# Kernel tuning notes

Measured on AMD Instinct MI355X. Metric: run time of the kernel, lower is better.

The kernel has to match this reference:

```python
import jax, jax.numpy as jnp
import numpy as np

NF, NX, GROUP_SIZE = 8192, 2048, 64
N_GROUPS = NX // GROUP_SIZE  # pad = 0 since NX % GROUP_SIZE == 0


def setup_inputs() -> dict:
    key = jax.random.key(0)
    k1, k2, k3, k4, k5 = jax.random.split(key, 5)
    x = jax.random.normal(k1, (4, 2048, NX), dtype=jnp.float32)
    packed = jax.random.randint(k2, (NF, NX // 2), 0, 256, dtype=jnp.int32)
    scales = jax.random.uniform(k3, (NF, N_GROUPS), dtype=jnp.float32)
    zeros = jax.random.randint(k4, (NF, N_GROUPS), 0, 16, dtype=jnp.int32)
    bias = jax.random.normal(k5, (NF,), dtype=jnp.float32)
    return {"x": x, "packed": packed, "scales": scales, "zeros": zeros, "bias": bias}


def _dequantize(packed, scales, zeros):
    # packed: [nf, nx//2] bytes, two int4 nibbles per byte (low nibble first)
    low = packed & 15
    high = (packed >> 4) & 15
    # interleave: q[:, 0::2] = low, q[:, 1::2] = high
    q = jnp.stack([low, high], axis=-1).reshape(NF, NX).astype(jnp.float32)
    q = q.reshape(NF, N_GROUPS, GROUP_SIZE)
    W = (q - zeros.astype(jnp.float32)[:, :, None]) * scales[:, :, None]
    return W.reshape(NF, NX)  # [nf, nx]


def reference(x, packed, scales, zeros, bias):
    W = _dequantize(packed, scales, zeros).astype(x.dtype)  # [nf, nx]
    size_out = x.shape[:-1] + (NF,)
    out = jnp.matmul(x.reshape(-1, NX), W.T) + bias  # addmm
    return out.reshape(size_out)
```

## Files before the change

kernel.cpp:

```cpp
#include <hip/hip_runtime.h>
#include <stdint.h>

#define NF 8192
#define NX 2048
#define MROWS 8192
#define NGROUPS 32
#define NSTEP 64

typedef unsigned short u16;
typedef __bf16 bf16x8 __attribute__((ext_vector_type(8)));
typedef float f32x4 __attribute__((ext_vector_type(4)));

#define AS1 __attribute__((address_space(1)))
#define AS3 __attribute__((address_space(3)))

__device__ __forceinline__ void glds16(const void* g, void* l) {
    __builtin_amdgcn_global_load_lds((AS1 void*)(uintptr_t)g,
                                     (AS3 void*)(uintptr_t)l, 16, 0, 0);
}

__device__ __forceinline__ u16 f2bf(float f) {
    unsigned u = __float_as_uint(f);
    return (u16)((u + 0x7FFFu + ((u >> 16) & 1u)) >> 16);
}

__global__ void dequant_kernel(const int* __restrict__ packed,
                               const float* __restrict__ scales,
                               const int* __restrict__ zeros,
                               uint32_t* __restrict__ W2) {
    int tid = blockIdx.x * blockDim.x + threadIdx.x;
    int f = tid >> 10;
    int i = tid & 1023;
    int g = f * NGROUPS + (i >> 5);
    int p = packed[tid];
    float s = scales[g];
    float z = (float)zeros[g];
    float w0 = ((float)(p & 15) - z) * s;
    float w1 = ((float)((p >> 4) & 15) - z) * s;
    W2[tid] = (uint32_t)f2bf(w0) | ((uint32_t)f2bf(w1) << 16);
}

__global__ void cvt_kernel(const float4* __restrict__ x, ushort4* __restrict__ y) {
    int i = blockIdx.x * blockDim.x + threadIdx.x;
    float4 v = x[i];
    ushort4 o;
    o.x = f2bf(v.x); o.y = f2bf(v.y); o.z = f2bf(v.z); o.w = f2bf(v.w);
    y[i] = o;
}


#define BAR    __builtin_amdgcn_s_barrier()
#define LGKM4  asm volatile("s_waitcnt lgkmcnt(4)" ::: "memory")
#define LGKM0  asm volatile("s_waitcnt lgkmcnt(0)" ::: "memory")
#define VMCNT6 asm volatile("s_waitcnt vmcnt(6)" ::: "memory")
#define VMCNT0 asm volatile("s_waitcnt vmcnt(0)" ::: "memory")
#define FENCE  __builtin_amdgcn_sched_barrier(0)

#define LD8(off) (*(const bf16x8*)(smem + (off)))

#define STAGE6(REG, S) do { \
    const char* _sa = srcA + (size_t)(S) * 64; \
    const char* _sb = srcB + (size_t)(S) * 64; \
    glds16(_sa,          smem + (REG) + t16); \
    glds16(_sa + 262144, smem + (REG) + 4096  + t16); \
    glds16(_sa + 524288, smem + (REG) + 8192  + t16); \
    glds16(_sa + 786432, smem + (REG) + 12288 + t16); \
    glds16(_sb,          smem + (REG) + 16384 + t16); \
    glds16(_sb + 262144, smem + (REG) + 20480 + t16); \
} while (0)

__global__ __launch_bounds__(256, 2)
void gemm_kernel(const u16* __restrict__ A, const u16* __restrict__ B,
                 const float* __restrict__ bias, float* __restrict__ C) {
    __shared__ __align__(16) char smem[73728];

    const int t = threadIdx.x;

    const int bid = blockIdx.x;
    const int xcd = bid & 7;
    const int local = bid >> 3;
    const int super = local >> 7;
    const int r = local & 127;
    const int by = xcd * 4 + super * 2 + (r & 1);
    const int bx = r >> 1;
    const int rowA0 = by * 256;
    const int rowB0 = bx * 128;

    const int t16 = t * 16;
    const int kslot = (t & 3) ^ ((t >> 3) & 3);
    const char* srcA = (const char*)A + (size_t)(rowA0 + (t >> 2)) * 4096 + kslot * 16;
    const char* srcB = (const char*)B + (size_t)(rowB0 + (t >> 2)) * 4096 + kslot * 16;

    const int lane = t & 63;
    const int wv = t >> 6;
    const int wm = wv >> 1;
    const int wn = wv & 1;
    const int l15 = lane & 15;
    const int quad = lane >> 4;
    const int uX = ((((l15 >> 1) & 3) ^ quad)) << 4;
    const int aOff = (wm * 128 + l15) * 64 + uX;
    const int bOff = 16384 + (wn * 64 + l15) * 64 + uX;

    f32x4 acc[8][4];
#pragma unroll
    for (int i = 0; i < 8; ++i)
#pragma unroll
        for (int j = 0; j < 4; ++j) acc[i][j] = {0.f, 0.f, 0.f, 0.f};

    bf16x8 a[8], b[4];

    STAGE6(0,     0);
    STAGE6(24576, 1);
    VMCNT6;

    int regC = 0, regN = 24576, regT = 49152;

#pragma unroll 1
    for (int s = 0; s < NSTEP; ++s) {
        FENCE; BAR; FENCE;
#pragma unroll
        for (int i = 0; i < 4; ++i) a[i] = LD8(regC + aOff + i * 1024);
#pragma unroll
        for (int j = 0; j < 4; ++j) b[j] = LD8(regC + bOff + j * 1024);
        FENCE;
#pragma unroll
        for (int i = 4; i < 8; ++i) a[i] = LD8(regC + aOff + i * 1024);
        if (s + 2 < NSTEP) STAGE6(regT, s + 2);
        FENCE; LGKM4; FENCE;
        __builtin_amdgcn_s_setprio(1);
#pragma unroll
        for (int i = 0; i < 4; ++i)
#pragma unroll
            for (int j = 0; j < 4; ++j)
                acc[i][j] = __builtin_amdgcn_mfma_f32_16x16x32_bf16(a[i], b[j], acc[i][j], 0, 0, 0);
        __builtin_amdgcn_s_setprio(0);
        FENCE; LGKM0; FENCE;
        __builtin_amdgcn_s_setprio(1);
#pragma unroll
        for (int i = 4; i < 8; ++i)
#pragma unroll
            for (int j = 0; j < 4; ++j)
                acc[i][j] = __builtin_amdgcn_mfma_f32_16x16x32_bf16(a[i], b[j], acc[i][j], 0, 0, 0);
        __builtin_amdgcn_s_setprio(0);
        FENCE;
        if (s + 2 < NSTEP) VMCNT6;
        else if (s + 1 < NSTEP) VMCNT0;

        const int tmp = regC; regC = regN; regN = regT; regT = tmp;
    }

    const int col0 = rowB0 + wn * 64 + l15;
    const int row0 = rowA0 + wm * 128 + quad * 4;
    float bj[4];
#pragma unroll
    for (int j = 0; j < 4; ++j) bj[j] = bias[col0 + j * 16];
#pragma unroll
    for (int i = 0; i < 8; ++i) {
#pragma unroll
        for (int e = 0; e < 4; ++e) {
            float* crow = C + (size_t)(row0 + i * 16 + e) * NF;
#pragma unroll
            for (int j = 0; j < 4; ++j)
                __builtin_nontemporal_store(acc[i][j][e] + bj[j], crow + col0 + j * 16);
        }
    }
}

extern "C" void kernel_launch(void* const* d_in, const int* in_sizes, int n_in,
                              void* d_out, int out_size, void* d_ws, size_t ws_size,
                              hipStream_t stream) {
    const float* x      = (const float*)d_in[0];
    const int* packed   = (const int*)d_in[1];
    const float* scales = (const float*)d_in[2];
    const int* zeros    = (const int*)d_in[3];
    const float* bias   = (const float*)d_in[4];
    float* out = (float*)d_out;

    u16* Wq = (u16*)d_ws;
    u16* Xb = Wq + (size_t)NF * NX;

    dequant_kernel<<<(NF * (NX / 2)) / 256, 256, 0, stream>>>(packed, scales, zeros, (uint32_t*)Wq);
    cvt_kernel<<<(MROWS * NX / 4) / 256, 256, 0, stream>>>((const float4*)x, (ushort4*)Xb);

    gemm_kernel<<<dim3((MROWS / 256) * (NF / 128)), 256, 0, stream>>>(Xb, Wq, bias, out);
}
```

Baseline: 305.7 us.

## Enlarge GEMM tile to 256x256 with 512 threads and K=64 double-buffered stages

The GEMM block tile grows from 256x128 to 256x256, run by 8 waves (512 threads) instead of 4. Each K stage now covers 64 elements using 128 KB of LDS with a new XOR swizzle, and the 3-deep pipeline becomes a 2-buffer ping-pong. The goal is more data reuse per LDS load and half as many barriers and K iterations. In exchange, LDS use rises to 128 KB per block, which likely drops occupancy to one block per CU, and the shallower prefetch exposes more global-load latency with a full vmcnt(0) wait every step.

```diff
diff --git a/kernel.cpp b/kernel.cpp
--- a/kernel.cpp
+++ b/kernel.cpp
@@ -5,7 +5,7 @@
 #define NX 2048
 #define MROWS 8192
 #define NGROUPS 32
-#define NSTEP 64
+#define NT 32
 
 typedef unsigned short u16;
 typedef __bf16 bf16x8 __attribute__((ext_vector_type(8)));
@@ -50,56 +50,60 @@
 
 
 #define BAR    __builtin_amdgcn_s_barrier()
-#define LGKM4  asm volatile("s_waitcnt lgkmcnt(4)" ::: "memory")
+#define LGKM8  asm volatile("s_waitcnt lgkmcnt(8)" ::: "memory")
 #define LGKM0  asm volatile("s_waitcnt lgkmcnt(0)" ::: "memory")
-#define VMCNT6 asm volatile("s_waitcnt vmcnt(6)" ::: "memory")
 #define VMCNT0 asm volatile("s_waitcnt vmcnt(0)" ::: "memory")
 #define FENCE  __builtin_amdgcn_sched_barrier(0)
 
 #define LD8(off) (*(const bf16x8*)(smem + (off)))
 
-#define STAGE6(REG, S) do { \
-    const char* _sa = srcA + (size_t)(S) * 64; \
-    const char* _sb = srcB + (size_t)(S) * 64; \
-    glds16(_sa,          smem + (REG) + t16); \
-    glds16(_sa + 262144, smem + (REG) + 4096  + t16); \
-    glds16(_sa + 524288, smem + (REG) + 8192  + t16); \
-    glds16(_sa + 786432, smem + (REG) + 12288 + t16); \
-    glds16(_sb,          smem + (REG) + 16384 + t16); \
-    glds16(_sb + 262144, smem + (REG) + 20480 + t16); \
+#define MFMA(d, va, vb) d = __builtin_amdgcn_mfma_f32_16x16x32_bf16(va, vb, d, 0, 0, 0)
+
+#define STAGE8(BUF, KOFF) do { \
+    glds16(srcA + (KOFF),          smem + (BUF) + t16); \
+    glds16(srcA + 262144 + (KOFF), smem + (BUF) + 8192  + t16); \
+    glds16(srcA + 524288 + (KOFF), smem + (BUF) + 16384 + t16); \
+    glds16(srcA + 786432 + (KOFF), smem + (BUF) + 24576 + t16); \
+    glds16(srcB + (KOFF),          smem + (BUF) + 32768 + t16); \
+    glds16(srcB + 262144 + (KOFF), smem + (BUF) + 40960 + t16); \
+    glds16(srcB + 524288 + (KOFF), smem + (BUF) + 49152 + t16); \
+    glds16(srcB + 786432 + (KOFF), smem + (BUF) + 57344 + t16); \
 } while (0)
 
-__global__ __launch_bounds__(256, 2)
+__global__ __launch_bounds__(512, 2)
 void gemm_kernel(const u16* __restrict__ A, const u16* __restrict__ B,
                  const float* __restrict__ bias, float* __restrict__ C) {
-    __shared__ __align__(16) char smem[73728];
+    __shared__ __align__(16) char smem[131072];
 
     const int t = threadIdx.x;
 
     const int bid = blockIdx.x;
     const int xcd = bid & 7;
     const int local = bid >> 3;
-    const int super = local >> 7;
-    const int r = local & 127;
+    const int super = local >> 6;
+    const int r = local & 63;
     const int by = xcd * 4 + super * 2 + (r & 1);
     const int bx = r >> 1;
     const int rowA0 = by * 256;
-    const int rowB0 = bx * 128;
+    const int rowB0 = bx * 256;
 
     const int t16 = t * 16;
-    const int kslot = (t & 3) ^ ((t >> 3) & 3);
-    const char* srcA = (const char*)A + (size_t)(rowA0 + (t >> 2)) * 4096 + kslot * 16;
-    const char* srcB = (const char*)B + (size_t)(rowB0 + (t >> 2)) * 4096 + kslot * 16;
+    const int ulog = (t & 7) ^ ((t >> 3) & 7);
+    const int koffS = (ulog >> 2) * 64 + (ulog & 3) * 16;
+    const char* srcA = (const char*)A + (size_t)(rowA0 + (t >> 3)) * 4096 + koffS;
+    const char* srcB = (const char*)B + (size_t)(rowB0 + (t >> 3)) * 4096 + koffS;
 
     const int lane = t & 63;
     const int wv = t >> 6;
-    const int wm = wv >> 1;
-    const int wn = wv & 1;
+    const int wm = wv >> 2;
+    const int wn = wv & 3;
     const int l15 = lane & 15;
     const int quad = lane >> 4;
-    const int uX = ((((l15 >> 1) & 3) ^ quad)) << 4;
-    const int aOff = (wm * 128 + l15) * 64 + uX;
-    const int bOff = 16384 + (wn * 64 + l15) * 64 + uX;
+    const int l7 = l15 & 7;
+    const int sx0 = (quad ^ l7) << 4;
+    const int sx1 = ((4 + quad) ^ l7) << 4;
+    const int aOff = (wm * 128 + l15) * 128;
+    const int bOff = 32768 + (wn * 64 + l15) * 128;
 
     f32x4 acc[8][4];
 #pragma unroll
@@ -107,46 +111,52 @@
 #pragma unroll
         for (int j = 0; j < 4; ++j) acc[i][j] = {0.f, 0.f, 0.f, 0.f};
 
-    bf16x8 a[8], b[4];
+    bf16x8 a0[8], a1[8], b0[4], b1[4];
 
-    STAGE6(0,     0);
-    STAGE6(24576, 1);
-    VMCNT6;
-
-    int regC = 0, regN = 24576, regT = 49152;
+    STAGE8(0, 0);
+    VMCNT0;
 
 #pragma unroll 1
-    for (int s = 0; s < NSTEP; ++s) {
+    for (int T = 0; T < NT; ++T) {
+        const int bo = (T & 1) << 16;
+        const int so = bo ^ 65536;
+
         FENCE; BAR; FENCE;
 #pragma unroll
-        for (int i = 0; i < 4; ++i) a[i] = LD8(regC + aOff + i * 1024);
+        for (int i = 0; i < 8; ++i) a0[i] = LD8(bo + aOff + i * 2048 + sx0);
 #pragma unroll
-        for (int j = 0; j < 4; ++j) b[j] = LD8(regC + bOff + j * 1024);
+        for (int j = 0; j < 4; ++j) b0[j] = LD8(bo + bOff + j * 2048 + sx0);
+        FENCE;
+        if (T + 1 < NT) STAGE8(so, (T + 1) * 128);
         FENCE;
 #pragma unroll
-        for (int i = 4; i < 8; ++i) a[i] = LD8(regC + aOff + i * 1024);
-        if (s + 2 < NSTEP) STAGE6(regT, s + 2);
-        FENCE; LGKM4; FENCE;
+        for (int i = 0; i < 8; ++i) a1[i] = LD8(bo + aOff + i * 2048 + sx1);
+        FENCE; LGKM8; FENCE;
         __builtin_amdgcn_s_setprio(1);
 #pragma unroll
-        for (int i = 0; i < 4; ++i)
+        for (int j = 0; j < 2; ++j)
 #pragma unroll
-            for (int j = 0; j < 4; ++j)
-                acc[i][j] = __builtin_amdgcn_mfma_f32_16x16x32_bf16(a[i], b[j], acc[i][j], 0, 0, 0);
+            for (int i = 0; i < 8; ++i) MFMA(acc[i][j], a0[i], b0[j]);
+        __builtin_amdgcn_s_setprio(0);
+        FENCE;
+#pragma unroll
+        for (int j = 0; j < 4; ++j) b1[j] = LD8(bo + bOff + j * 2048 + sx1);
+        FENCE;
+        __builtin_amdgcn_s_setprio(1);
+#pragma unroll
+        for (int j = 2; j < 4; ++j)
+#pragma unroll
+            for (int i = 0; i < 8; ++i) MFMA(acc[i][j], a0[i], b0[j]);
         __builtin_amdgcn_s_setprio(0);
         FENCE; LGKM0; FENCE;
         __builtin_amdgcn_s_setprio(1);
 #pragma unroll
-        for (int i = 4; i < 8; ++i)
+        for (int j = 0; j < 4; ++j)
 #pragma unroll
-            for (int j = 0; j < 4; ++j)
-                acc[i][j] = __builtin_amdgcn_mfma_f32_16x16x32_bf16(a[i], b[j], acc[i][j], 0, 0, 0);
+            for (int i = 0; i < 8; ++i) MFMA(acc[i][j], a1[i], b1[j]);
         __builtin_amdgcn_s_setprio(0);
         FENCE;
-        if (s + 2 < NSTEP) VMCNT6;
-        else if (s + 1 < NSTEP) VMCNT0;
-
-        const int tmp = regC; regC = regN; regN = regT; regT = tmp;
+        if (T + 1 < NT) VMCNT0;
     }
 
     const int col0 = rowB0 + wn * 64 + l15;
@@ -182,5 +192,5 @@
     dequant_kernel<<<(NF * (NX / 2)) / 256, 256, 0, stream>>>(packed, scales, zeros, (uint32_t*)Wq);
     cvt_kernel<<<(MROWS * NX / 4) / 256, 256, 0, stream>>>((const float4*)x, (ushort4*)Xb);
 
-    gemm_kernel<<<dim3((MROWS / 256) * (NF / 128)), 256, 0, stream>>>(Xb, Wq, bias, out);
+    gemm_kernel<<<dim3((MROWS / 256) * (NF / 256)), 512, 0, stream>>>(Xb, Wq, bias, out);
 }
```

Result: faster. 284.5 us (-6.9%).
